# Optimization experiments

Measured on AMD Instinct MI355X. Metric: run time of the kernel, lower is better.

## Reference

```python
import jax, jax.numpy as jnp
import numpy as np

N = 100000
E = 3200000
F_IN = 512
HID = 16
C = 40


def setup_inputs() -> dict:
    key = jax.random.key(0)
    ks = jax.random.split(key, 6)
    x = jax.random.normal(ks[0], (N, F_IN), dtype=jnp.float32)
    edge_index = jax.random.randint(ks[1], (2, E), 0, N, dtype=jnp.int64)
    edge_weight = jax.random.uniform(ks[2], (E,), dtype=jnp.float32)
    # Glorot-style init like PyG GCNConv
    W1 = jax.random.normal(ks[3], (F_IN, HID), dtype=jnp.float32) * (1.0 / np.sqrt(F_IN))
    b1 = jnp.zeros((HID,), dtype=jnp.float32)
    W2 = jax.random.normal(ks[4], (HID, C), dtype=jnp.float32) * (1.0 / np.sqrt(HID))
    b2 = jnp.zeros((C,), dtype=jnp.float32)
    return {"x": x, "edge_index": edge_index, "edge_weight": edge_weight,
            "W1": W1, "b1": b1, "W2": W2, "b2": b2}


def _gcn_conv(h, W, b, row, col, norm, num_nodes):
    # h: [N, Fin] -> [N, Fout];  out = D^-1/2 A D^-1/2 (h W) + b, no self loops
    h = h @ W                                           # [N, Fout]
    msg = norm[:, None] * h[row]                        # gather + scale, [E, Fout]
    agg = jax.ops.segment_sum(msg, col, num_segments=num_nodes)  # scatter-add
    return agg + b


def reference(x, edge_index, edge_weight, W1, b1, W2, b2):
    num_nodes = x.shape[0]
    row, col = edge_index[0], edge_index[1]
    # symmetric gcn normalization (add_self_loops=False)
    deg = jax.ops.segment_sum(edge_weight, col, num_segments=num_nodes)  # [N]
    deg_inv_sqrt = jnp.where(deg > 0, jax.lax.rsqrt(jnp.maximum(deg, 1e-30)), 0.0)
    norm = deg_inv_sqrt[row] * edge_weight * deg_inv_sqrt[col]           # [E]

    h = jax.nn.relu(_gcn_conv(x, W1, b1, row, col, norm, num_nodes))
    # dropout is identity in eval mode (training=False)
    h = _gcn_conv(h, W2, b2, row, col, norm, num_nodes)
    return jax.nn.log_softmax(h, axis=-1)
```

## Files before the change

kernel.cpp:

```cpp
#include <hip/hip_runtime.h>

typedef float floatx4_t __attribute__((ext_vector_type(4)));
typedef __bf16 bf16x8_t __attribute__((ext_vector_type(8)));
typedef short shortx8_t __attribute__((ext_vector_type(8)));
typedef unsigned long long ull;

__device__ __forceinline__ unsigned short f2bf_rne(float f) {
    unsigned u = __float_as_uint(f);
    unsigned r = u + 0x7FFFu + ((u >> 16) & 1u);
    return (unsigned short)(r >> 16);
}
__device__ __forceinline__ float bf2f(unsigned short h) {
    return __uint_as_float((unsigned)h << 16);
}

#define MAXB 2048
#define CHUNK 8192
#define CAP 3072

__global__ __launch_bounds__(256) void k_scatter(const int* __restrict__ row,
                                                 const int* __restrict__ col,
                                                 const float* __restrict__ ew,
                                                 int* __restrict__ gcnt,
                                                 ull* __restrict__ packed,
                                                 int E, int B) {
    __shared__ int h[MAXB];
    __shared__ int base[MAXB];
    int t = threadIdx.x;
    for (int i = t; i < B; i += 256) h[i] = 0;
    __syncthreads();
    int cbase = blockIdx.x * CHUNK;
#pragma unroll 2
    for (int k = 0; k < 8; ++k) {
        int e = cbase + k * 1024 + t * 4;
        if (e + 3 < E) {
            int4 c4 = *(const int4*)(col + e);
            atomicAdd(&h[c4.x >> 6], 1);
            atomicAdd(&h[c4.y >> 6], 1);
            atomicAdd(&h[c4.z >> 6], 1);
            atomicAdd(&h[c4.w >> 6], 1);
        } else {
            for (int j = 0; j < 4; ++j)
                if (e + j < E) atomicAdd(&h[col[e + j] >> 6], 1);
        }
    }
    __syncthreads();
    for (int i = t; i < B; i += 256) {
        int c = h[i];
        base[i] = c ? atomicAdd(&gcnt[i], c) : 0;
    }
    __syncthreads();
#pragma unroll 2
    for (int k = 0; k < 8; ++k) {
        int e = cbase + k * 1024 + t * 4;
        if (e + 3 < E) {
            int4 c4 = *(const int4*)(col + e);
            int4 r4 = *(const int4*)(row + e);
            float4 w4 = *(const float4*)(ew + e);
            int cs[4] = {c4.x, c4.y, c4.z, c4.w};
            int rs[4] = {r4.x, r4.y, r4.z, r4.w};
            float wsv[4] = {w4.x, w4.y, w4.z, w4.w};
#pragma unroll
            for (int j = 0; j < 4; ++j) {
                int c = cs[j];
                int b = c >> 6;
                int pos = atomicAdd(&base[b], 1);
                if (pos < CAP) {
                    ull hi = (ull)(unsigned)((rs[j] << 6) | (c & 63)) << 32;
                    packed[(size_t)b * CAP + pos] = hi | (unsigned)__float_as_uint(wsv[j]);
                }
            }
        } else {
            for (int j = 0; j < 4; ++j) {
                if (e + j < E) {
                    int c = col[e + j];
                    int b = c >> 6;
                    int pos = atomicAdd(&base[b], 1);
                    if (pos < CAP) {
                        ull hi = (ull)(unsigned)((row[e + j] << 6) | (c & 63)) << 32;
                        packed[(size_t)b * CAP + pos] = hi | (unsigned)__float_as_uint(ew[e + j]);
                    }
                }
            }
        }
    }
}

__global__ __launch_bounds__(256) void k_sortgemm(const int* __restrict__ gcnt,
                                                  const ull* __restrict__ packed,
                                                  unsigned* __restrict__ packed2,
                                                  int2* __restrict__ rng,
                                                  float* __restrict__ dis,
                                                  const float* __restrict__ x,
                                                  const float* __restrict__ W1,
                                                  unsigned short* __restrict__ h1s, int N) {
    __shared__ int cnt[64];
    __shared__ int cur[64];
    __shared__ float dacc[64];
    __shared__ float sdis[64];
    int t = threadIdx.x;
    if (t < 64) { cnt[t] = 0; dacc[t] = 0.f; }
    __syncthreads();
    int b = blockIdx.x;
    size_t gbase = (size_t)b * CAP;
    int szr = gcnt[b];
    int sz = szr < CAP ? szr : CAP;

    for (int j = t; j < sz; j += 256) {
        ull p = packed[gbase + j];
        int nd = (int)(p >> 32) & 63;
        atomicAdd(&cnt[nd], 1);
        atomicAdd(&dacc[nd], __uint_as_float((unsigned)p));
    }
    __syncthreads();
    if (t < 64) {
        int c = cnt[t];
        int xp = c;
#pragma unroll
        for (int off = 1; off < 64; off <<= 1) {
            int y = __shfl_up(xp, off);
            if (t >= off) xp += y;
        }
        int off0 = xp - c;
        cur[t] = off0;
        float s = dacc[t];
        float d = (s > 0.f) ? rsqrtf(s) : 0.f;
        sdis[t] = d;
        int g = b * 64 + t;
        if (g < N) {
            rng[g] = make_int2((int)gbase + off0, (int)gbase + off0 + c);
            dis[g] = d;
        }
    }
    __syncthreads();
    for (int j = t; j < sz; j += 256) {
        ull p = packed[gbase + j];
        int nd = (int)(p >> 32) & 63;
        int r = (int)(p >> 32) >> 6;
        unsigned short wb = f2bf_rne(__uint_as_float((unsigned)p));
        int pos = atomicAdd(&cur[nd], 1);
        packed2[gbase + pos] = ((unsigned)r << 15) | (unsigned)wb;
    }

    const int lane = t & 63;
    const int wave = t >> 6;
    const int m = lane & 15;
    const int q = lane >> 4;
    const int nbase = b * 64 + wave * 16;

    shortx8_t bs[16];
#pragma unroll
    for (int c = 0; c < 16; ++c) {
#pragma unroll
        for (int j = 0; j < 8; ++j) {
            int k = c * 32 + q * 8 + j;
            bs[c][j] = (short)f2bf_rne(W1[k * 16 + m]);
        }
    }

    int rowi = nbase + m;
    if (rowi >= N) rowi = N - 1;
    const float* xr = x + (size_t)rowi * 512;

    floatx4_t acc = {0.f, 0.f, 0.f, 0.f};
#pragma unroll
    for (int c = 0; c < 16; ++c) {
        const float4 u0 = *(const float4*)(xr + c * 32 + q * 8);
        const float4 u1 = *(const float4*)(xr + c * 32 + q * 8 + 4);
        shortx8_t as;
        as[0] = (short)f2bf_rne(u0.x); as[1] = (short)f2bf_rne(u0.y);
        as[2] = (short)f2bf_rne(u0.z); as[3] = (short)f2bf_rne(u0.w);
        as[4] = (short)f2bf_rne(u1.x); as[5] = (short)f2bf_rne(u1.y);
        as[6] = (short)f2bf_rne(u1.z); as[7] = (short)f2bf_rne(u1.w);
        acc = __builtin_amdgcn_mfma_f32_16x16x32_bf16(
            __builtin_bit_cast(bf16x8_t, as),
            __builtin_bit_cast(bf16x8_t, bs[c]), acc, 0, 0, 0);
    }

#pragma unroll
    for (int r = 0; r < 4; ++r) {
        int node = nbase + q * 4 + r;
        if (node < N)
            h1s[(size_t)node * 16 + m] = f2bf_rne(acc[r] * sdis[wave * 16 + q * 4 + r]);
    }
}

__global__ __launch_bounds__(256) void k_agg1(const int2* __restrict__ rng,
                                              const unsigned* __restrict__ packed2,
                                              const float* __restrict__ dis,
                                              const unsigned short* __restrict__ h1s,
                                              const float* __restrict__ b1,
                                              unsigned short* __restrict__ hs, int N) {
    int wv = (blockIdx.x * 256 + threadIdx.x) >> 6;
    if (wv >= N) return;
    int lane = threadIdx.x & 63;
    int e4 = lane >> 4, f = lane & 15;
    int2 r2 = rng[wv];
    int beg = r2.x, end = r2.y;
    float a0 = 0.f, a1 = 0.f;
    int i = beg + e4;
    for (; i + 4 < end; i += 8) {
        unsigned p0 = packed2[i];
        unsigned p1 = packed2[i + 4];
        int r0 = p0 >> 15, r1 = p1 >> 15;
        a0 += __uint_as_float((p0 & 0x7FFFu) << 16) * bf2f(h1s[(size_t)r0 * 16 + f]);
        a1 += __uint_as_float((p1 & 0x7FFFu) << 16) * bf2f(h1s[(size_t)r1 * 16 + f]);
    }
    if (i < end) {
        unsigned p = packed2[i];
        int r = p >> 15;
        a0 += __uint_as_float((p & 0x7FFFu) << 16) * bf2f(h1s[(size_t)r * 16 + f]);
    }
    float a = a0 + a1;
    a += __shfl_xor(a, 16);
    a += __shfl_xor(a, 32);
    if (e4 == 0) {
        float dg = dis[wv];
        float v = dg * a + b1[f];
        v = (v > 0.f) ? v : 0.f;
        hs[(size_t)wv * 16 + f] = f2bf_rne(dg * v);
    }
}

__global__ __launch_bounds__(256) void k_agg2out(const int2* __restrict__ rng,
                                                 const unsigned* __restrict__ packed2,
                                                 const float* __restrict__ dis,
                                                 const unsigned short* __restrict__ hs,
                                                 const float* __restrict__ W2,
                                                 const float* __restrict__ b2,
                                                 float* __restrict__ out, int N) {
    int wv = (blockIdx.x * 256 + threadIdx.x) >> 6;
    if (wv >= N) return;
    int lane = threadIdx.x & 63;
    int e4 = lane >> 4, f = lane & 15;
    int2 r2 = rng[wv];
    int beg = r2.x, end = r2.y;
    float a0 = 0.f, a1 = 0.f;
    int i = beg + e4;
    for (; i + 4 < end; i += 8) {
        unsigned p0 = packed2[i];
        unsigned p1 = packed2[i + 4];
        int r0 = p0 >> 15, r1 = p1 >> 15;
        a0 += __uint_as_float((p0 & 0x7FFFu) << 16) * bf2f(hs[(size_t)r0 * 16 + f]);
        a1 += __uint_as_float((p1 & 0x7FFFu) << 16) * bf2f(hs[(size_t)r1 * 16 + f]);
    }
    if (i < end) {
        unsigned p = packed2[i];
        int r = p >> 15;
        a0 += __uint_as_float((p & 0x7FFFu) << 16) * bf2f(hs[(size_t)r * 16 + f]);
    }
    float a = a0 + a1;
    a += __shfl_xor(a, 16);
    a += __shfl_xor(a, 32);

    float dg = dis[wv];
    int c = lane;
    int cc = (c < 40) ? c : 39;
    float z = 0.f;
#pragma unroll
    for (int fi = 0; fi < 16; ++fi) {
        float af = __shfl(a, fi);
        z += af * W2[fi * 40 + cc];
    }
    z = dg * z + b2[cc];

    float zm = (c < 40) ? z : -3.4e38f;
#pragma unroll
    for (int off = 1; off < 64; off <<= 1) zm = fmaxf(zm, __shfl_xor(zm, off));
    float ex = (c < 40) ? __expf(z - zm) : 0.f;
    float s = ex;
#pragma unroll
    for (int off = 1; off < 64; off <<= 1) s += __shfl_xor(s, off);
    float lse = zm + __logf(s);
    if (c < 40) out[(size_t)wv * 40 + c] = z - lse;
}

extern "C" void kernel_launch(void* const* d_in, const int* in_sizes, int n_in,
                              void* d_out, int out_size, void* d_ws, size_t ws_size,
                              hipStream_t stream) {
    const float* x  = (const float*)d_in[0];
    const int*   ei = (const int*)d_in[1];
    const float* ew = (const float*)d_in[2];
    const float* W1 = (const float*)d_in[3];
    const float* b1 = (const float*)d_in[4];
    const float* W2 = (const float*)d_in[5];
    const float* b2 = (const float*)d_in[6];

    const int N = in_sizes[0] / 512;
    const int E = in_sizes[2];
    const int* row = ei;
    const int* col = ei + E;
    const int B = (N + 63) >> 6;

    ull*      packed  = (ull*)d_ws;
    unsigned* packed2 = (unsigned*)(packed + (size_t)B * CAP);
    int*      gcnt    = (int*)(packed2 + (size_t)B * CAP);
    int2*     rng     = (int2*)(gcnt + B + (B & 1));
    float*    dis     = (float*)(rng + N);
    unsigned short* h1s = (unsigned short*)(dis + N);
    unsigned short* hs  = h1s + (size_t)16 * N;

    hipMemsetAsync(gcnt, 0, (size_t)B * sizeof(int), stream);

    const int gC = (E + CHUNK - 1) / CHUNK;
    const int gW = (N * 64 + 255) / 256;

    k_scatter<<<gC, 256, 0, stream>>>(row, col, ew, gcnt, packed, E, B);
    k_sortgemm<<<B, 256, 0, stream>>>(gcnt, packed, packed2, rng, dis, x, W1, h1s, N);
    k_agg1<<<gW, 256, 0, stream>>>(rng, packed2, dis, h1s, b1, hs, N);
    k_agg2out<<<gW, 256, 0, stream>>>(rng, packed2, dis, hs, W2, b2, (float*)d_out, N);
}
```

Before: 531.6 us.

## Replace bucket sort with per-node fixed-capacity edge slots via global atomics

The two-level bucket sort goes away: the 64-node bucket scatter plus the in-block counting sort that built CSR ranges. Each edge now claims a slot in a fixed 96-entry per-node array through a global atomic counter, and the weighted degree is accumulated with a global float atomic. The GEMM kernel no longer does sorting passes and only computes the inverse-sqrt degree. The aim is to cut a full read and rewrite of the edge list and the shared-memory sort work. In exchange it adds two random global atomics per edge and a padded, sparser edge layout. Edges beyond 96 per node are silently dropped.

```diff
diff --git a/kernel.cpp b/kernel.cpp
--- a/kernel.cpp
+++ b/kernel.cpp
@@ -3,7 +3,8 @@
 typedef float floatx4_t __attribute__((ext_vector_type(4)));
 typedef __bf16 bf16x8_t __attribute__((ext_vector_type(8)));
 typedef short shortx8_t __attribute__((ext_vector_type(8)));
-typedef unsigned long long ull;
+
+#define CAP 96
 
 __device__ __forceinline__ unsigned short f2bf_rne(float f) {
     unsigned u = __float_as_uint(f);
@@ -14,133 +15,60 @@
     return __uint_as_float((unsigned)h << 16);
 }
 
-#define MAXB 2048
-#define CHUNK 8192
-#define CAP 3072
-
 __global__ __launch_bounds__(256) void k_scatter(const int* __restrict__ row,
                                                  const int* __restrict__ col,
                                                  const float* __restrict__ ew,
-                                                 int* __restrict__ gcnt,
-                                                 ull* __restrict__ packed,
-                                                 int E, int B) {
-    __shared__ int h[MAXB];
-    __shared__ int base[MAXB];
-    int t = threadIdx.x;
-    for (int i = t; i < B; i += 256) h[i] = 0;
-    __syncthreads();
-    int cbase = blockIdx.x * CHUNK;
-#pragma unroll 2
-    for (int k = 0; k < 8; ++k) {
-        int e = cbase + k * 1024 + t * 4;
-        if (e + 3 < E) {
-            int4 c4 = *(const int4*)(col + e);
-            atomicAdd(&h[c4.x >> 6], 1);
-            atomicAdd(&h[c4.y >> 6], 1);
-            atomicAdd(&h[c4.z >> 6], 1);
-            atomicAdd(&h[c4.w >> 6], 1);
-        } else {
-            for (int j = 0; j < 4; ++j)
-                if (e + j < E) atomicAdd(&h[col[e + j] >> 6], 1);
+                                                 int* __restrict__ cnt,
+                                                 float* __restrict__ degw,
+                                                 unsigned* __restrict__ packed2,
+                                                 int E) {
+    int e = (blockIdx.x * 256 + threadIdx.x) * 4;
+    if (e + 3 < E) {
+        int4 c4 = *(const int4*)(col + e);
+        int4 r4 = *(const int4*)(row + e);
+        float4 w4 = *(const float4*)(ew + e);
+        int cs[4] = {c4.x, c4.y, c4.z, c4.w};
+        int rs[4] = {r4.x, r4.y, r4.z, r4.w};
+        float ws[4] = {w4.x, w4.y, w4.z, w4.w};
+#pragma unroll
+        for (int j = 0; j < 4; ++j) {
+            int c = cs[j];
+            int pos = atomicAdd(&cnt[c], 1);
+            atomicAdd(&degw[c], ws[j]);
+            if (pos < CAP)
+                packed2[(size_t)c * CAP + pos] =
+                    ((unsigned)rs[j] << 15) | (unsigned)f2bf_rne(ws[j]);
         }
-    }
-    __syncthreads();
-    for (int i = t; i < B; i += 256) {
-        int c = h[i];
-        base[i] = c ? atomicAdd(&gcnt[i], c) : 0;
-    }
-    __syncthreads();
-#pragma unroll 2
-    for (int k = 0; k < 8; ++k) {
-        int e = cbase + k * 1024 + t * 4;
-        if (e + 3 < E) {
-            int4 c4 = *(const int4*)(col + e);
-            int4 r4 = *(const int4*)(row + e);
-            float4 w4 = *(const float4*)(ew + e);
-            int cs[4] = {c4.x, c4.y, c4.z, c4.w};
-            int rs[4] = {r4.x, r4.y, r4.z, r4.w};
-            float wsv[4] = {w4.x, w4.y, w4.z, w4.w};
-#pragma unroll
-            for (int j = 0; j < 4; ++j) {
-                int c = cs[j];
-                int b = c >> 6;
-                int pos = atomicAdd(&base[b], 1);
-                if (pos < CAP) {
-                    ull hi = (ull)(unsigned)((rs[j] << 6) | (c & 63)) << 32;
-                    packed[(size_t)b * CAP + pos] = hi | (unsigned)__float_as_uint(wsv[j]);
-                }
-            }
-        } else {
-            for (int j = 0; j < 4; ++j) {
-                if (e + j < E) {
-                    int c = col[e + j];
-                    int b = c >> 6;
-                    int pos = atomicAdd(&base[b], 1);
-                    if (pos < CAP) {
-                        ull hi = (ull)(unsigned)((row[e + j] << 6) | (c & 63)) << 32;
-                        packed[(size_t)b * CAP + pos] = hi | (unsigned)__float_as_uint(ew[e + j]);
-                    }
-                }
+    } else {
+        for (int j = 0; j < 4; ++j) {
+            if (e + j < E) {
+                int c = col[e + j];
+                int pos = atomicAdd(&cnt[c], 1);
+                atomicAdd(&degw[c], ew[e + j]);
+                if (pos < CAP)
+                    packed2[(size_t)c * CAP + pos] =
+                        ((unsigned)row[e + j] << 15) | (unsigned)f2bf_rne(ew[e + j]);
             }
         }
     }
 }
 
-__global__ __launch_bounds__(256) void k_sortgemm(const int* __restrict__ gcnt,
-                                                  const ull* __restrict__ packed,
-                                                  unsigned* __restrict__ packed2,
-                                                  int2* __restrict__ rng,
-                                                  float* __restrict__ dis,
-                                                  const float* __restrict__ x,
-                                                  const float* __restrict__ W1,
-                                                  unsigned short* __restrict__ h1s, int N) {
-    __shared__ int cnt[64];
-    __shared__ int cur[64];
-    __shared__ float dacc[64];
+__global__ __launch_bounds__(256) void k_gemmdis(const float* __restrict__ degw,
+                                                 float* __restrict__ dis,
+                                                 const float* __restrict__ x,
+                                                 const float* __restrict__ W1,
+                                                 unsigned short* __restrict__ h1s, int N) {
     __shared__ float sdis[64];
     int t = threadIdx.x;
-    if (t < 64) { cnt[t] = 0; dacc[t] = 0.f; }
-    __syncthreads();
     int b = blockIdx.x;
-    size_t gbase = (size_t)b * CAP;
-    int szr = gcnt[b];
-    int sz = szr < CAP ? szr : CAP;
-
-    for (int j = t; j < sz; j += 256) {
-        ull p = packed[gbase + j];
-        int nd = (int)(p >> 32) & 63;
-        atomicAdd(&cnt[nd], 1);
-        atomicAdd(&dacc[nd], __uint_as_float((unsigned)p));
-    }
-    __syncthreads();
     if (t < 64) {
-        int c = cnt[t];
-        int xp = c;
-#pragma unroll
-        for (int off = 1; off < 64; off <<= 1) {
-            int y = __shfl_up(xp, off);
-            if (t >= off) xp += y;
-        }
-        int off0 = xp - c;
-        cur[t] = off0;
-        float s = dacc[t];
+        int g = b * 64 + t;
+        float s = (g < N) ? degw[g] : 0.f;
         float d = (s > 0.f) ? rsqrtf(s) : 0.f;
         sdis[t] = d;
-        int g = b * 64 + t;
-        if (g < N) {
-            rng[g] = make_int2((int)gbase + off0, (int)gbase + off0 + c);
-            dis[g] = d;
-        }
+        if (g < N) dis[g] = d;
     }
     __syncthreads();
-    for (int j = t; j < sz; j += 256) {
-        ull p = packed[gbase + j];
-        int nd = (int)(p >> 32) & 63;
-        int r = (int)(p >> 32) >> 6;
-        unsigned short wb = f2bf_rne(__uint_as_float((unsigned)p));
-        int pos = atomicAdd(&cur[nd], 1);
-        packed2[gbase + pos] = ((unsigned)r << 15) | (unsigned)wb;
-    }
 
     const int lane = t & 63;
     const int wave = t >> 6;
@@ -185,7 +113,7 @@
     }
 }
 
-__global__ __launch_bounds__(256) void k_agg1(const int2* __restrict__ rng,
+__global__ __launch_bounds__(256) void k_agg1(const int* __restrict__ cnt,
                                               const unsigned* __restrict__ packed2,
                                               const float* __restrict__ dis,
                                               const unsigned short* __restrict__ h1s,
@@ -195,8 +123,9 @@
     if (wv >= N) return;
     int lane = threadIdx.x & 63;
     int e4 = lane >> 4, f = lane & 15;
-    int2 r2 = rng[wv];
-    int beg = r2.x, end = r2.y;
+    int c = cnt[wv];
+    if (c > CAP) c = CAP;
+    int beg = wv * CAP, end = beg + c;
     float a0 = 0.f, a1 = 0.f;
     int i = beg + e4;
     for (; i + 4 < end; i += 8) {
@@ -222,7 +151,7 @@
     }
 }
 
-__global__ __launch_bounds__(256) void k_agg2out(const int2* __restrict__ rng,
+__global__ __launch_bounds__(256) void k_agg2out(const int* __restrict__ cnt,
                                                  const unsigned* __restrict__ packed2,
                                                  const float* __restrict__ dis,
                                                  const unsigned short* __restrict__ hs,
@@ -233,8 +162,9 @@
     if (wv >= N) return;
     int lane = threadIdx.x & 63;
     int e4 = lane >> 4, f = lane & 15;
-    int2 r2 = rng[wv];
-    int beg = r2.x, end = r2.y;
+    int cn = cnt[wv];
+    if (cn > CAP) cn = CAP;
+    int beg = wv * CAP, end = beg + cn;
     float a0 = 0.f, a1 = 0.f;
     int i = beg + e4;
     for (; i + 4 < end; i += 8) {
@@ -291,22 +221,22 @@
     const int* row = ei;
     const int* col = ei + E;
     const int B = (N + 63) >> 6;
-
-    ull*      packed  = (ull*)d_ws;
-    unsigned* packed2 = (unsigned*)(packed + (size_t)B * CAP);
-    int*      gcnt    = (int*)(packed2 + (size_t)B * CAP);
-    int2*     rng     = (int2*)(gcnt + B + (B & 1));
-    float*    dis     = (float*)(rng + N);
-    unsigned short* h1s = (unsigned short*)(dis + N);
-    unsigned short* hs  = h1s + (size_t)16 * N;
-
-    hipMemsetAsync(gcnt, 0, (size_t)B * sizeof(int), stream);
-
-    const int gC = (E + CHUNK - 1) / CHUNK;
+    const int Npad = B * 64;
+
+    unsigned* packed2 = (unsigned*)d_ws;
+    int*      cnt     = (int*)(packed2 + (size_t)Npad * CAP);
+    float*    degw    = (float*)(cnt + Npad);
+    float*    dis     = degw + Npad;
+    unsigned short* h1s = (unsigned short*)(dis + Npad);
+    unsigned short* hs  = h1s + (size_t)16 * Npad;
+
+    hipMemsetAsync(cnt, 0, (size_t)Npad * 2 * sizeof(int), stream);
+
+    const int gS = (E + 1023) / 1024;
     const int gW = (N * 64 + 255) / 256;
 
-    k_scatter<<<gC, 256, 0, stream>>>(row, col, ew, gcnt, packed, E, B);
-    k_sortgemm<<<B, 256, 0, stream>>>(gcnt, packed, packed2, rng, dis, x, W1, h1s, N);
-    k_agg1<<<gW, 256, 0, stream>>>(rng, packed2, dis, h1s, b1, hs, N);
-    k_agg2out<<<gW, 256, 0, stream>>>(rng, packed2, dis, hs, W2, b2, (float*)d_out, N);
-}
+    k_scatter<<<gS, 256, 0, stream>>>(row, col, ew, cnt, degw, packed2, E);
+    k_gemmdis<<<B, 256, 0, stream>>>(degw, dis, x, W1, h1s, N);
+    k_agg1<<<gW, 256, 0, stream>>>(cnt, packed2, dis, h1s, b1, hs, N);
+    k_agg2out<<<gW, 256, 0, stream>>>(cnt, packed2, dis, hs, W2, b2, (float*)d_out, N);
+}
```

Result: slower. 762.1 us (+43.3%).

## Drop per-node sort; aggregate bucket edges via LDS atomics per 64-node block

Applied to the files above, without the earlier changes.

The per-bucket counting sort into a compact packed2 CSR array is removed. The aggregation kernels now process each 64-node bucket's unsorted packed edges directly, accumulating into a shared-memory [64][17] tile with LDS float atomics. Degree sums move into the scatter kernel as global float atomics. This removes a full pass over the packed edges and the packed2 writes, in exchange for many global atomics on degw and LDS atomic contention. It also reads 8-byte packed entries with fp32 weights instead of 4-byte bf16-weight entries.

```diff
diff --git a/kernel.cpp b/kernel.cpp
--- a/kernel.cpp
+++ b/kernel.cpp
@@ -22,6 +22,7 @@
                                                  const int* __restrict__ col,
                                                  const float* __restrict__ ew,
                                                  int* __restrict__ gcnt,
+                                                 float* __restrict__ degw,
                                                  ull* __restrict__ packed,
                                                  int E, int B) {
     __shared__ int h[MAXB];
@@ -65,6 +66,7 @@
                 int c = cs[j];
                 int b = c >> 6;
                 int pos = atomicAdd(&base[b], 1);
+                atomicAdd(&degw[c], wsv[j]);
                 if (pos < CAP) {
                     ull hi = (ull)(unsigned)((rs[j] << 6) | (c & 63)) << 32;
                     packed[(size_t)b * CAP + pos] = hi | (unsigned)__float_as_uint(wsv[j]);
@@ -76,6 +78,7 @@
                     int c = col[e + j];
                     int b = c >> 6;
                     int pos = atomicAdd(&base[b], 1);
+                    atomicAdd(&degw[c], ew[e + j]);
                     if (pos < CAP) {
                         ull hi = (ull)(unsigned)((row[e + j] << 6) | (c & 63)) << 32;
                         packed[(size_t)b * CAP + pos] = hi | (unsigned)__float_as_uint(ew[e + j]);
@@ -86,61 +89,22 @@
     }
 }
 
-__global__ __launch_bounds__(256) void k_sortgemm(const int* __restrict__ gcnt,
-                                                  const ull* __restrict__ packed,
-                                                  unsigned* __restrict__ packed2,
-                                                  int2* __restrict__ rng,
-                                                  float* __restrict__ dis,
-                                                  const float* __restrict__ x,
-                                                  const float* __restrict__ W1,
-                                                  unsigned short* __restrict__ h1s, int N) {
-    __shared__ int cnt[64];
-    __shared__ int cur[64];
-    __shared__ float dacc[64];
+__global__ __launch_bounds__(256) void k_gemmdis(const float* __restrict__ degw,
+                                                 float* __restrict__ dis,
+                                                 const float* __restrict__ x,
+                                                 const float* __restrict__ W1,
+                                                 unsigned short* __restrict__ h1s, int N) {
     __shared__ float sdis[64];
     int t = threadIdx.x;
-    if (t < 64) { cnt[t] = 0; dacc[t] = 0.f; }
-    __syncthreads();
     int b = blockIdx.x;
-    size_t gbase = (size_t)b * CAP;
-    int szr = gcnt[b];
-    int sz = szr < CAP ? szr : CAP;
-
-    for (int j = t; j < sz; j += 256) {
-        ull p = packed[gbase + j];
-        int nd = (int)(p >> 32) & 63;
-        atomicAdd(&cnt[nd], 1);
-        atomicAdd(&dacc[nd], __uint_as_float((unsigned)p));
-    }
-    __syncthreads();
     if (t < 64) {
-        int c = cnt[t];
-        int xp = c;
-#pragma unroll
-        for (int off = 1; off < 64; off <<= 1) {
-            int y = __shfl_up(xp, off);
-            if (t >= off) xp += y;
-        }
-        int off0 = xp - c;
-        cur[t] = off0;
-        float s = dacc[t];
+        int g = b * 64 + t;
+        float s = (g < N) ? degw[g] : 0.f;
         float d = (s > 0.f) ? rsqrtf(s) : 0.f;
         sdis[t] = d;
-        int g = b * 64 + t;
-        if (g < N) {
-            rng[g] = make_int2((int)gbase + off0, (int)gbase + off0 + c);
-            dis[g] = d;
-        }
-    }
-    __syncthreads();
-    for (int j = t; j < sz; j += 256) {
-        ull p = packed[gbase + j];
-        int nd = (int)(p >> 32) & 63;
-        int r = (int)(p >> 32) >> 6;
-        unsigned short wb = f2bf_rne(__uint_as_float((unsigned)p));
-        int pos = atomicAdd(&cur[nd], 1);
-        packed2[gbase + pos] = ((unsigned)r << 15) | (unsigned)wb;
-    }
+        if (g < N) dis[g] = d;
+    }
+    __syncthreads();
 
     const int lane = t & 63;
     const int wave = t >> 6;
@@ -185,94 +149,114 @@
     }
 }
 
-__global__ __launch_bounds__(256) void k_agg1(const int2* __restrict__ rng,
-                                              const unsigned* __restrict__ packed2,
+__global__ __launch_bounds__(256) void k_agg1(const int* __restrict__ gcnt,
+                                              const ull* __restrict__ packed,
                                               const float* __restrict__ dis,
                                               const unsigned short* __restrict__ h1s,
                                               const float* __restrict__ b1,
                                               unsigned short* __restrict__ hs, int N) {
-    int wv = (blockIdx.x * 256 + threadIdx.x) >> 6;
-    if (wv >= N) return;
-    int lane = threadIdx.x & 63;
-    int e4 = lane >> 4, f = lane & 15;
-    int2 r2 = rng[wv];
-    int beg = r2.x, end = r2.y;
-    float a0 = 0.f, a1 = 0.f;
-    int i = beg + e4;
-    for (; i + 4 < end; i += 8) {
-        unsigned p0 = packed2[i];
-        unsigned p1 = packed2[i + 4];
-        int r0 = p0 >> 15, r1 = p1 >> 15;
-        a0 += __uint_as_float((p0 & 0x7FFFu) << 16) * bf2f(h1s[(size_t)r0 * 16 + f]);
-        a1 += __uint_as_float((p1 & 0x7FFFu) << 16) * bf2f(h1s[(size_t)r1 * 16 + f]);
-    }
-    if (i < end) {
-        unsigned p = packed2[i];
-        int r = p >> 15;
-        a0 += __uint_as_float((p & 0x7FFFu) << 16) * bf2f(h1s[(size_t)r * 16 + f]);
-    }
-    float a = a0 + a1;
-    a += __shfl_xor(a, 16);
-    a += __shfl_xor(a, 32);
-    if (e4 == 0) {
-        float dg = dis[wv];
-        float v = dg * a + b1[f];
-        v = (v > 0.f) ? v : 0.f;
-        hs[(size_t)wv * 16 + f] = f2bf_rne(dg * v);
-    }
-}
-
-__global__ __launch_bounds__(256) void k_agg2out(const int2* __restrict__ rng,
-                                                 const unsigned* __restrict__ packed2,
+    __shared__ float acc[64][17];
+    int t = threadIdx.x;
+    for (int k = t; k < 64 * 17; k += 256) ((float*)acc)[k] = 0.f;
+    __syncthreads();
+    int b = blockIdx.x;
+    size_t gbase = (size_t)b * CAP;
+    int szr = gcnt[b];
+    int sz = szr < CAP ? szr : CAP;
+
+    int f = t & 15, slot = t >> 4;
+    int j = slot;
+    for (; j + 16 < sz; j += 32) {
+        ull p0 = packed[gbase + j];
+        ull p1 = packed[gbase + j + 16];
+        int hi0 = (int)(p0 >> 32), hi1 = (int)(p1 >> 32);
+        float v0 = __uint_as_float((unsigned)p0) * bf2f(h1s[(size_t)(hi0 >> 6) * 16 + f]);
+        float v1 = __uint_as_float((unsigned)p1) * bf2f(h1s[(size_t)(hi1 >> 6) * 16 + f]);
+        atomicAdd(&acc[hi0 & 63][f], v0);
+        atomicAdd(&acc[hi1 & 63][f], v1);
+    }
+    for (; j < sz; j += 16) {
+        ull p = packed[gbase + j];
+        int hi = (int)(p >> 32);
+        float v = __uint_as_float((unsigned)p) * bf2f(h1s[(size_t)(hi >> 6) * 16 + f]);
+        atomicAdd(&acc[hi & 63][f], v);
+    }
+    __syncthreads();
+
+    for (int k = t; k < 1024; k += 256) {
+        int n = k >> 4, ff = k & 15;
+        int node = b * 64 + n;
+        if (node < N) {
+            float dg = dis[node];
+            float v = dg * acc[n][ff] + b1[ff];
+            v = (v > 0.f) ? v : 0.f;
+            hs[(size_t)node * 16 + ff] = f2bf_rne(dg * v);
+        }
+    }
+}
+
+__global__ __launch_bounds__(256) void k_agg2out(const int* __restrict__ gcnt,
+                                                 const ull* __restrict__ packed,
                                                  const float* __restrict__ dis,
                                                  const unsigned short* __restrict__ hs,
                                                  const float* __restrict__ W2,
                                                  const float* __restrict__ b2,
                                                  float* __restrict__ out, int N) {
-    int wv = (blockIdx.x * 256 + threadIdx.x) >> 6;
-    if (wv >= N) return;
-    int lane = threadIdx.x & 63;
-    int e4 = lane >> 4, f = lane & 15;
-    int2 r2 = rng[wv];
-    int beg = r2.x, end = r2.y;
-    float a0 = 0.f, a1 = 0.f;
-    int i = beg + e4;
-    for (; i + 4 < end; i += 8) {
-        unsigned p0 = packed2[i];
-        unsigned p1 = packed2[i + 4];
-        int r0 = p0 >> 15, r1 = p1 >> 15;
-        a0 += __uint_as_float((p0 & 0x7FFFu) << 16) * bf2f(hs[(size_t)r0 * 16 + f]);
-        a1 += __uint_as_float((p1 & 0x7FFFu) << 16) * bf2f(hs[(size_t)r1 * 16 + f]);
-    }
-    if (i < end) {
-        unsigned p = packed2[i];
-        int r = p >> 15;
-        a0 += __uint_as_float((p & 0x7FFFu) << 16) * bf2f(hs[(size_t)r * 16 + f]);
-    }
-    float a = a0 + a1;
-    a += __shfl_xor(a, 16);
-    a += __shfl_xor(a, 32);
-
-    float dg = dis[wv];
+    __shared__ float acc[64][17];
+    __shared__ float w2s[640];
+    __shared__ float b2s[40];
+    int t = threadIdx.x;
+    for (int k = t; k < 64 * 17; k += 256) ((float*)acc)[k] = 0.f;
+    for (int k = t; k < 640; k += 256) w2s[k] = W2[k];
+    if (t < 40) b2s[t] = b2[t];
+    __syncthreads();
+    int b = blockIdx.x;
+    size_t gbase = (size_t)b * CAP;
+    int szr = gcnt[b];
+    int sz = szr < CAP ? szr : CAP;
+
+    int f = t & 15, slot = t >> 4;
+    int j = slot;
+    for (; j + 16 < sz; j += 32) {
+        ull p0 = packed[gbase + j];
+        ull p1 = packed[gbase + j + 16];
+        int hi0 = (int)(p0 >> 32), hi1 = (int)(p1 >> 32);
+        float v0 = __uint_as_float((unsigned)p0) * bf2f(hs[(size_t)(hi0 >> 6) * 16 + f]);
+        float v1 = __uint_as_float((unsigned)p1) * bf2f(hs[(size_t)(hi1 >> 6) * 16 + f]);
+        atomicAdd(&acc[hi0 & 63][f], v0);
+        atomicAdd(&acc[hi1 & 63][f], v1);
+    }
+    for (; j < sz; j += 16) {
+        ull p = packed[gbase + j];
+        int hi = (int)(p >> 32);
+        float v = __uint_as_float((unsigned)p) * bf2f(hs[(size_t)(hi >> 6) * 16 + f]);
+        atomicAdd(&acc[hi & 63][f], v);
+    }
+    __syncthreads();
+
+    int lane = t & 63, wave = t >> 6;
     int c = lane;
     int cc = (c < 40) ? c : 39;
-    float z = 0.f;
-#pragma unroll
-    for (int fi = 0; fi < 16; ++fi) {
-        float af = __shfl(a, fi);
-        z += af * W2[fi * 40 + cc];
-    }
-    z = dg * z + b2[cc];
-
-    float zm = (c < 40) ? z : -3.4e38f;
-#pragma unroll
-    for (int off = 1; off < 64; off <<= 1) zm = fmaxf(zm, __shfl_xor(zm, off));
-    float ex = (c < 40) ? __expf(z - zm) : 0.f;
-    float s = ex;
-#pragma unroll
-    for (int off = 1; off < 64; off <<= 1) s += __shfl_xor(s, off);
-    float lse = zm + __logf(s);
-    if (c < 40) out[(size_t)wv * 40 + c] = z - lse;
+    for (int ni = 0; ni < 16; ++ni) {
+        int n = wave * 16 + ni;
+        int node = b * 64 + n;
+        if (node >= N) continue;
+        float z = 0.f;
+#pragma unroll
+        for (int fi = 0; fi < 16; ++fi) z += acc[n][fi] * w2s[fi * 40 + cc];
+        float dg = dis[node];
+        z = dg * z + b2s[cc];
+
+        float zm = (c < 40) ? z : -3.4e38f;
+#pragma unroll
+        for (int off = 1; off < 64; off <<= 1) zm = fmaxf(zm, __shfl_xor(zm, off));
+        float ex = (c < 40) ? __expf(z - zm) : 0.f;
+        float s = ex;
+#pragma unroll
+        for (int off = 1; off < 64; off <<= 1) s += __shfl_xor(s, off);
+        float lse = zm + __logf(s);
+        if (c < 40) out[(size_t)node * 40 + c] = z - lse;
+    }
 }
 
 extern "C" void kernel_launch(void* const* d_in, const int* in_sizes, int n_in,
@@ -291,22 +275,21 @@
     const int* row = ei;
     const int* col = ei + E;
     const int B = (N + 63) >> 6;
-
-    ull*      packed  = (ull*)d_ws;
-    unsigned* packed2 = (unsigned*)(packed + (size_t)B * CAP);
-    int*      gcnt    = (int*)(packed2 + (size_t)B * CAP);
-    int2*     rng     = (int2*)(gcnt + B + (B & 1));
-    float*    dis     = (float*)(rng + N);
-    unsigned short* h1s = (unsigned short*)(dis + N);
-    unsigned short* hs  = h1s + (size_t)16 * N;
-
-    hipMemsetAsync(gcnt, 0, (size_t)B * sizeof(int), stream);
+    const int Npad = B * 64;
+
+    ull*      packed = (ull*)d_ws;
+    int*      gcnt   = (int*)(packed + (size_t)B * CAP);
+    float*    degw   = (float*)(gcnt + B);
+    float*    dis    = degw + Npad;
+    unsigned short* h1s = (unsigned short*)(dis + Npad);
+    unsigned short* hs  = h1s + (size_t)16 * Npad;
+
+    hipMemsetAsync(gcnt, 0, ((size_t)B + Npad) * sizeof(int), stream);
 
     const int gC = (E + CHUNK - 1) / CHUNK;
-    const int gW = (N * 64 + 255) / 256;
-
-    k_scatter<<<gC, 256, 0, stream>>>(row, col, ew, gcnt, packed, E, B);
-    k_sortgemm<<<B, 256, 0, stream>>>(gcnt, packed, packed2, rng, dis, x, W1, h1s, N);
-    k_agg1<<<gW, 256, 0, stream>>>(rng, packed2, dis, h1s, b1, hs, N);
-    k_agg2out<<<gW, 256, 0, stream>>>(rng, packed2, dis, hs, W2, b2, (float*)d_out, N);
-}
+
+    k_scatter<<<gC, 256, 0, stream>>>(row, col, ew, gcnt, degw, packed, E, B);
+    k_gemmdis<<<B, 256, 0, stream>>>(degw, dis, x, W1, h1s, N);
+    k_agg1<<<B, 256, 0, stream>>>(gcnt, packed, dis, h1s, b1, hs, N);
+    k_agg2out<<<B, 256, 0, stream>>>(gcnt, packed, dis, hs, W2, b2, (float*)d_out, N);
+}
```

Measured after the change: 1.130 ms. 113% more time.

## Run GEMM concurrently with edge scatter and apply source normalization during aggregation

Applied to the files above, without the earlier changes.

The dense x@W1 GEMM moves out of the sort kernel into extra blocks of the scatter kernel, so the bandwidth-heavy read of x overlaps with the edge bucketing. Because the source-degree scaling is no longer known when the GEMM runs, both aggregation kernels now multiply each gathered row by dis[row] per edge, and the ReLU output is stored unscaled. The aggregation loops are also unrolled to four accumulators for more memory-level parallelism. In exchange, every edge does an extra random gather of dis, and the scatter kernel's shared-memory footprint now applies to the GEMM blocks too.

```diff
diff --git a/kernel.cpp b/kernel.cpp
--- a/kernel.cpp
+++ b/kernel.cpp
@@ -18,86 +18,130 @@
 #define CHUNK 8192
 #define CAP 3072
 
-__global__ __launch_bounds__(256) void k_scatter(const int* __restrict__ row,
-                                                 const int* __restrict__ col,
-                                                 const float* __restrict__ ew,
-                                                 int* __restrict__ gcnt,
-                                                 ull* __restrict__ packed,
-                                                 int E, int B) {
-    __shared__ int h[MAXB];
-    __shared__ int base[MAXB];
+__global__ __launch_bounds__(256) void k_scatter_gemm(const int* __restrict__ row,
+                                                      const int* __restrict__ col,
+                                                      const float* __restrict__ ew,
+                                                      int* __restrict__ gcnt,
+                                                      ull* __restrict__ packed,
+                                                      const float* __restrict__ x,
+                                                      const float* __restrict__ W1,
+                                                      unsigned short* __restrict__ h1s,
+                                                      int E, int B, int gC, int N) {
     int t = threadIdx.x;
-    for (int i = t; i < B; i += 256) h[i] = 0;
-    __syncthreads();
-    int cbase = blockIdx.x * CHUNK;
+    if ((int)blockIdx.x < gC) {
+        __shared__ int h[MAXB];
+        __shared__ int base[MAXB];
+        for (int i = t; i < B; i += 256) h[i] = 0;
+        __syncthreads();
+        int cbase = blockIdx.x * CHUNK;
 #pragma unroll 2
-    for (int k = 0; k < 8; ++k) {
-        int e = cbase + k * 1024 + t * 4;
-        if (e + 3 < E) {
-            int4 c4 = *(const int4*)(col + e);
-            atomicAdd(&h[c4.x >> 6], 1);
-            atomicAdd(&h[c4.y >> 6], 1);
-            atomicAdd(&h[c4.z >> 6], 1);
-            atomicAdd(&h[c4.w >> 6], 1);
-        } else {
-            for (int j = 0; j < 4; ++j)
-                if (e + j < E) atomicAdd(&h[col[e + j] >> 6], 1);
-        }
-    }
-    __syncthreads();
-    for (int i = t; i < B; i += 256) {
-        int c = h[i];
-        base[i] = c ? atomicAdd(&gcnt[i], c) : 0;
-    }
-    __syncthreads();
+        for (int k = 0; k < 8; ++k) {
+            int e = cbase + k * 1024 + t * 4;
+            if (e + 3 < E) {
+                int4 c4 = *(const int4*)(col + e);
+                atomicAdd(&h[c4.x >> 6], 1);
+                atomicAdd(&h[c4.y >> 6], 1);
+                atomicAdd(&h[c4.z >> 6], 1);
+                atomicAdd(&h[c4.w >> 6], 1);
+            } else {
+                for (int j = 0; j < 4; ++j)
+                    if (e + j < E) atomicAdd(&h[col[e + j] >> 6], 1);
+            }
+        }
+        __syncthreads();
+        for (int i = t; i < B; i += 256) {
+            int c = h[i];
+            base[i] = c ? atomicAdd(&gcnt[i], c) : 0;
+        }
+        __syncthreads();
 #pragma unroll 2
-    for (int k = 0; k < 8; ++k) {
-        int e = cbase + k * 1024 + t * 4;
-        if (e + 3 < E) {
-            int4 c4 = *(const int4*)(col + e);
-            int4 r4 = *(const int4*)(row + e);
-            float4 w4 = *(const float4*)(ew + e);
-            int cs[4] = {c4.x, c4.y, c4.z, c4.w};
-            int rs[4] = {r4.x, r4.y, r4.z, r4.w};
-            float wsv[4] = {w4.x, w4.y, w4.z, w4.w};
-#pragma unroll
-            for (int j = 0; j < 4; ++j) {
-                int c = cs[j];
-                int b = c >> 6;
-                int pos = atomicAdd(&base[b], 1);
-                if (pos < CAP) {
-                    ull hi = (ull)(unsigned)((rs[j] << 6) | (c & 63)) << 32;
-                    packed[(size_t)b * CAP + pos] = hi | (unsigned)__float_as_uint(wsv[j]);
-                }
-            }
-        } else {
-            for (int j = 0; j < 4; ++j) {
-                if (e + j < E) {
-                    int c = col[e + j];
+        for (int k = 0; k < 8; ++k) {
+            int e = cbase + k * 1024 + t * 4;
+            if (e + 3 < E) {
+                int4 c4 = *(const int4*)(col + e);
+                int4 r4 = *(const int4*)(row + e);
+                float4 w4 = *(const float4*)(ew + e);
+                int cs[4] = {c4.x, c4.y, c4.z, c4.w};
+                int rs[4] = {r4.x, r4.y, r4.z, r4.w};
+                float wsv[4] = {w4.x, w4.y, w4.z, w4.w};
+#pragma unroll
+                for (int j = 0; j < 4; ++j) {
+                    int c = cs[j];
                     int b = c >> 6;
                     int pos = atomicAdd(&base[b], 1);
                     if (pos < CAP) {
-                        ull hi = (ull)(unsigned)((row[e + j] << 6) | (c & 63)) << 32;
-                        packed[(size_t)b * CAP + pos] = hi | (unsigned)__float_as_uint(ew[e + j]);
+                        ull hi = (ull)(unsigned)((rs[j] << 6) | (c & 63)) << 32;
+                        packed[(size_t)b * CAP + pos] = hi | (unsigned)__float_as_uint(wsv[j]);
+                    }
+                }
+            } else {
+                for (int j = 0; j < 4; ++j) {
+                    if (e + j < E) {
+                        int c = col[e + j];
+                        int b = c >> 6;
+                        int pos = atomicAdd(&base[b], 1);
+                        if (pos < CAP) {
+                            ull hi = (ull)(unsigned)((row[e + j] << 6) | (c & 63)) << 32;
+                            packed[(size_t)b * CAP + pos] = hi | (unsigned)__float_as_uint(ew[e + j]);
+                        }
                     }
                 }
             }
         }
-    }
-}
-
-__global__ __launch_bounds__(256) void k_sortgemm(const int* __restrict__ gcnt,
-                                                  const ull* __restrict__ packed,
-                                                  unsigned* __restrict__ packed2,
-                                                  int2* __restrict__ rng,
-                                                  float* __restrict__ dis,
-                                                  const float* __restrict__ x,
-                                                  const float* __restrict__ W1,
-                                                  unsigned short* __restrict__ h1s, int N) {
+    } else {
+        int b = blockIdx.x - gC;
+        const int lane = t & 63;
+        const int wave = t >> 6;
+        const int m = lane & 15;
+        const int q = lane >> 4;
+        const int nbase = b * 64 + wave * 16;
+
+        shortx8_t bs[16];
+#pragma unroll
+        for (int c = 0; c < 16; ++c) {
+#pragma unroll
+            for (int j = 0; j < 8; ++j) {
+                int k = c * 32 + q * 8 + j;
+                bs[c][j] = (short)f2bf_rne(W1[k * 16 + m]);
+            }
+        }
+
+        int rowi = nbase + m;
+        if (rowi >= N) rowi = N - 1;
+        const float* xr = x + (size_t)rowi * 512;
+
+        floatx4_t acc = {0.f, 0.f, 0.f, 0.f};
+#pragma unroll
+        for (int c = 0; c < 16; ++c) {
+            const float4 u0 = *(const float4*)(xr + c * 32 + q * 8);
+            const float4 u1 = *(const float4*)(xr + c * 32 + q * 8 + 4);
+            shortx8_t as;
+            as[0] = (short)f2bf_rne(u0.x); as[1] = (short)f2bf_rne(u0.y);
+            as[2] = (short)f2bf_rne(u0.z); as[3] = (short)f2bf_rne(u0.w);
+            as[4] = (short)f2bf_rne(u1.x); as[5] = (short)f2bf_rne(u1.y);
+            as[6] = (short)f2bf_rne(u1.z); as[7] = (short)f2bf_rne(u1.w);
+            acc = __builtin_amdgcn_mfma_f32_16x16x32_bf16(
+                __builtin_bit_cast(bf16x8_t, as),
+                __builtin_bit_cast(bf16x8_t, bs[c]), acc, 0, 0, 0);
+        }
+
+#pragma unroll
+        for (int r = 0; r < 4; ++r) {
+            int node = nbase + q * 4 + r;
+            if (node < N)
+                h1s[(size_t)node * 16 + m] = f2bf_rne(acc[r]);
+        }
+    }
+}
+
+__global__ __launch_bounds__(256) void k_sortdis(const int* __restrict__ gcnt,
+                                                 const ull* __restrict__ packed,
+                                                 unsigned* __restrict__ packed2,
+                                                 int2* __restrict__ rng,
+                                                 float* __restrict__ dis, int N) {
     __shared__ int cnt[64];
     __shared__ int cur[64];
     __shared__ float dacc[64];
-    __shared__ float sdis[64];
     int t = threadIdx.x;
     if (t < 64) { cnt[t] = 0; dacc[t] = 0.f; }
     __syncthreads();
@@ -125,7 +169,6 @@
         cur[t] = off0;
         float s = dacc[t];
         float d = (s > 0.f) ? rsqrtf(s) : 0.f;
-        sdis[t] = d;
         int g = b * 64 + t;
         if (g < N) {
             rng[g] = make_int2((int)gbase + off0, (int)gbase + off0 + c);
@@ -140,48 +183,6 @@
         unsigned short wb = f2bf_rne(__uint_as_float((unsigned)p));
         int pos = atomicAdd(&cur[nd], 1);
         packed2[gbase + pos] = ((unsigned)r << 15) | (unsigned)wb;
-    }
-
-    const int lane = t & 63;
-    const int wave = t >> 6;
-    const int m = lane & 15;
-    const int q = lane >> 4;
-    const int nbase = b * 64 + wave * 16;
-
-    shortx8_t bs[16];
-#pragma unroll
-    for (int c = 0; c < 16; ++c) {
-#pragma unroll
-        for (int j = 0; j < 8; ++j) {
-            int k = c * 32 + q * 8 + j;
-            bs[c][j] = (short)f2bf_rne(W1[k * 16 + m]);
-        }
-    }
-
-    int rowi = nbase + m;
-    if (rowi >= N) rowi = N - 1;
-    const float* xr = x + (size_t)rowi * 512;
-
-    floatx4_t acc = {0.f, 0.f, 0.f, 0.f};
-#pragma unroll
-    for (int c = 0; c < 16; ++c) {
-        const float4 u0 = *(const float4*)(xr + c * 32 + q * 8);
-        const float4 u1 = *(const float4*)(xr + c * 32 + q * 8 + 4);
-        shortx8_t as;
-        as[0] = (short)f2bf_rne(u0.x); as[1] = (short)f2bf_rne(u0.y);
-        as[2] = (short)f2bf_rne(u0.z); as[3] = (short)f2bf_rne(u0.w);
-        as[4] = (short)f2bf_rne(u1.x); as[5] = (short)f2bf_rne(u1.y);
-        as[6] = (short)f2bf_rne(u1.z); as[7] = (short)f2bf_rne(u1.w);
-        acc = __builtin_amdgcn_mfma_f32_16x16x32_bf16(
-            __builtin_bit_cast(bf16x8_t, as),
-            __builtin_bit_cast(bf16x8_t, bs[c]), acc, 0, 0, 0);
-    }
-
-#pragma unroll
-    for (int r = 0; r < 4; ++r) {
-        int node = nbase + q * 4 + r;
-        if (node < N)
-            h1s[(size_t)node * 16 + m] = f2bf_rne(acc[r] * sdis[wave * 16 + q * 4 + r]);
     }
 }
 
@@ -197,28 +198,32 @@
     int e4 = lane >> 4, f = lane & 15;
     int2 r2 = rng[wv];
     int beg = r2.x, end = r2.y;
-    float a0 = 0.f, a1 = 0.f;
+    float a0 = 0.f, a1 = 0.f, a2 = 0.f, a3 = 0.f;
     int i = beg + e4;
-    for (; i + 4 < end; i += 8) {
+    for (; i + 12 < end; i += 16) {
         unsigned p0 = packed2[i];
         unsigned p1 = packed2[i + 4];
-        int r0 = p0 >> 15, r1 = p1 >> 15;
-        a0 += __uint_as_float((p0 & 0x7FFFu) << 16) * bf2f(h1s[(size_t)r0 * 16 + f]);
-        a1 += __uint_as_float((p1 & 0x7FFFu) << 16) * bf2f(h1s[(size_t)r1 * 16 + f]);
-    }
-    if (i < end) {
+        unsigned p2 = packed2[i + 8];
+        unsigned p3 = packed2[i + 12];
+        int r0 = p0 >> 15, r1 = p1 >> 15, r2i = p2 >> 15, r3 = p3 >> 15;
+        a0 += __uint_as_float((p0 & 0x7FFFu) << 16) * dis[r0] * bf2f(h1s[(size_t)r0 * 16 + f]);
+        a1 += __uint_as_float((p1 & 0x7FFFu) << 16) * dis[r1] * bf2f(h1s[(size_t)r1 * 16 + f]);
+        a2 += __uint_as_float((p2 & 0x7FFFu) << 16) * dis[r2i] * bf2f(h1s[(size_t)r2i * 16 + f]);
+        a3 += __uint_as_float((p3 & 0x7FFFu) << 16) * dis[r3] * bf2f(h1s[(size_t)r3 * 16 + f]);
+    }
+    for (; i < end; i += 4) {
         unsigned p = packed2[i];
         int r = p >> 15;
-        a0 += __uint_as_float((p & 0x7FFFu) << 16) * bf2f(h1s[(size_t)r * 16 + f]);
-    }
-    float a = a0 + a1;
+        a0 += __uint_as_float((p & 0x7FFFu) << 16) * dis[r] * bf2f(h1s[(size_t)r * 16 + f]);
+    }
+    float a = (a0 + a1) + (a2 + a3);
     a += __shfl_xor(a, 16);
     a += __shfl_xor(a, 32);
     if (e4 == 0) {
         float dg = dis[wv];
         float v = dg * a + b1[f];
         v = (v > 0.f) ? v : 0.f;
-        hs[(size_t)wv * 16 + f] = f2bf_rne(dg * v);
+        hs[(size_t)wv * 16 + f] = f2bf_rne(v);
     }
 }
 
@@ -235,21 +240,25 @@
     int e4 = lane >> 4, f = lane & 15;
     int2 r2 = rng[wv];
     int beg = r2.x, end = r2.y;
-    float a0 = 0.f, a1 = 0.f;
+    float a0 = 0.f, a1 = 0.f, a2 = 0.f, a3 = 0.f;
     int i = beg + e4;
-    for (; i + 4 < end; i += 8) {
+    for (; i + 12 < end; i += 16) {
         unsigned p0 = packed2[i];
         unsigned p1 = packed2[i + 4];
-        int r0 = p0 >> 15, r1 = p1 >> 15;
-        a0 += __uint_as_float((p0 & 0x7FFFu) << 16) * bf2f(hs[(size_t)r0 * 16 + f]);
-        a1 += __uint_as_float((p1 & 0x7FFFu) << 16) * bf2f(hs[(size_t)r1 * 16 + f]);
-    }
-    if (i < end) {
+        unsigned p2 = packed2[i + 8];
+        unsigned p3 = packed2[i + 12];
+        int r0 = p0 >> 15, r1 = p1 >> 15, r2i = p2 >> 15, r3 = p3 >> 15;
+        a0 += __uint_as_float((p0 & 0x7FFFu) << 16) * dis[r0] * bf2f(hs[(size_t)r0 * 16 + f]);
+        a1 += __uint_as_float((p1 & 0x7FFFu) << 16) * dis[r1] * bf2f(hs[(size_t)r1 * 16 + f]);
+        a2 += __uint_as_float((p2 & 0x7FFFu) << 16) * dis[r2i] * bf2f(hs[(size_t)r2i * 16 + f]);
+        a3 += __uint_as_float((p3 & 0x7FFFu) << 16) * dis[r3] * bf2f(hs[(size_t)r3 * 16 + f]);
+    }
+    for (; i < end; i += 4) {
         unsigned p = packed2[i];
         int r = p >> 15;
-        a0 += __uint_as_float((p & 0x7FFFu) << 16) * bf2f(hs[(size_t)r * 16 + f]);
-    }
-    float a = a0 + a1;
+        a0 += __uint_as_float((p & 0x7FFFu) << 16) * dis[r] * bf2f(hs[(size_t)r * 16 + f]);
+    }
+    float a = (a0 + a1) + (a2 + a3);
     a += __shfl_xor(a, 16);
     a += __shfl_xor(a, 32);
 
@@ -305,8 +314,9 @@
     const int gC = (E + CHUNK - 1) / CHUNK;
     const int gW = (N * 64 + 255) / 256;
 
-    k_scatter<<<gC, 256, 0, stream>>>(row, col, ew, gcnt, packed, E, B);
-    k_sortgemm<<<B, 256, 0, stream>>>(gcnt, packed, packed2, rng, dis, x, W1, h1s, N);
+    k_scatter_gemm<<<gC + B, 256, 0, stream>>>(row, col, ew, gcnt, packed,
+                                               x, W1, h1s, E, B, gC, N);
+    k_sortdis<<<B, 256, 0, stream>>>(gcnt, packed, packed2, rng, dis, N);
     k_agg1<<<gW, 256, 0, stream>>>(rng, packed2, dis, h1s, b1, hs, N);
     k_agg2out<<<gW, 256, 0, stream>>>(rng, packed2, dis, hs, W2, b2, (float*)d_out, N);
 }
```

New measurement: 512.7 us. -3.6%, faster.
